# Kernel optimization log

Hardware: AMD Instinct MI355X
Metric: run time of the kernel (lower is better)

Reference implementation:

```python
import jax, jax.numpy as jnp
import numpy as np

ALPHA = 0.2  # LeakyReLU negative slope (args.alpha)

def _leaky(x):
    return jnp.where(x >= 0, x, ALPHA * x)

def setup_inputs() -> dict:
    key = jax.random.key(0)
    k1, k2, k3, k4 = jax.random.split(key, 4)
    B, N, F_in, F_out = 4, 2048, 512, 512
    h = jax.random.normal(k1, (B, N, F_in), dtype=jnp.float32)
    W = jax.random.normal(k2, (F_in, F_out), dtype=jnp.float32) * 0.05
    a = jax.random.normal(k3, (2 * F_out, 1), dtype=jnp.float32) * 0.05
    adj = jax.random.randint(k4, (B, N, N), 0, 2, dtype=jnp.int32)
    return {"h": h, "W": W, "a": a, "adj": adj}

def reference(h, W, a, adj):
    F_out = W.shape[1]
    Wh = jnp.matmul(h, W)                      # [B, N, F_out]
    # a_input is built under torch.no_grad() in the original -> stop_gradient
    Wh_sg = jax.lax.stop_gradient(Wh)
    a1 = a[:F_out, 0]                          # score for node i (repeat_interleave side)
    a2 = a[F_out:, 0]                          # score for node j (repeat side)
    s_i = Wh_sg @ a1                           # [B, N]
    s_j = Wh_sg @ a2                           # [B, N]
    e = _leaky(s_i[:, :, None] + s_j[:, None, :])   # [B, N, N]
    e = jnp.where(adj > 0, e, jnp.float32(-9e15))
    attention = jax.nn.softmax(e, axis=1)      # softmax over dim=1, as in original
    # dropout skipped (eval mode, training=False)
    h_prime = jnp.einsum('bij,bjf->bif', attention, Wh)
    return _leaky(h_prime)                     # concat=True
```

## Files before the change

### kernel.cpp

```cpp
#include <hip/hip_runtime.h>

#define BB 4
#define NN 2048
#define FF 512
#define ALPHA 0.2f

typedef unsigned short u16;
typedef unsigned int u32;
typedef __attribute__((ext_vector_type(8))) short bf16x8;
typedef __attribute__((ext_vector_type(4))) float f32x4;

__device__ __forceinline__ u16 f2bf(float x) {
  union { float f; u32 u; } v; v.f = x;
  u32 r = v.u + 0x7fffu + ((v.u >> 16) & 1u);
  return (u16)(r >> 16);
}
__device__ __forceinline__ float leaky(float x) { return x >= 0.f ? x : ALPHA * x; }

__global__ __launch_bounds__(256) void k_wa(const float* __restrict__ W,
                                            const float* __restrict__ a,
                                            float* __restrict__ wa1,
                                            float* __restrict__ wa2) {
  const int wave = threadIdx.x >> 6, lane = threadIdx.x & 63;
  const int k = blockIdx.x * 4 + wave;
  const int f0 = lane * 8;
  float4 w0 = *(const float4*)(W + (size_t)k * FF + f0);
  float4 w1 = *(const float4*)(W + (size_t)k * FF + f0 + 4);
  float4 p0 = *(const float4*)(a + f0);
  float4 p1 = *(const float4*)(a + f0 + 4);
  float4 q0 = *(const float4*)(a + FF + f0);
  float4 q1 = *(const float4*)(a + FF + f0 + 4);
  float d1 = w0.x*p0.x + w0.y*p0.y + w0.z*p0.z + w0.w*p0.w
           + w1.x*p1.x + w1.y*p1.y + w1.z*p1.z + w1.w*p1.w;
  float d2 = w0.x*q0.x + w0.y*q0.y + w0.z*q0.z + w0.w*q0.w
           + w1.x*q1.x + w1.y*q1.y + w1.z*q1.z + w1.w*q1.w;
#pragma unroll
  for (int o = 32; o; o >>= 1) { d1 += __shfl_xor(d1, o); d2 += __shfl_xor(d2, o); }
  if (lane == 0) { wa1[k] = d1; wa2[k] = d2; }
}

__global__ __launch_bounds__(256) void k_wt(const float* __restrict__ W,
                                            u16* __restrict__ wt) {
  __shared__ float T[64][65];
  const int k0 = blockIdx.x * 64, f0 = blockIdx.y * 64;
  const int tid = threadIdx.x;
  const int c = tid & 15, r0 = tid >> 4;
#pragma unroll
  for (int p = 0; p < 4; p++) {
    const int k = r0 + p * 16;
    float4 v = *(const float4*)(W + (size_t)(k0 + k) * FF + f0 + c * 4);
    T[c * 4 + 0][k] = v.x;
    T[c * 4 + 1][k] = v.y;
    T[c * 4 + 2][k] = v.z;
    T[c * 4 + 3][k] = v.w;
  }
  __syncthreads();
  const int kc = tid & 7, fr0 = tid >> 3;
#pragma unroll
  for (int p = 0; p < 2; p++) {
    const int f = fr0 + p * 32;
    union { uint4 q; u16 s[8]; } o;
#pragma unroll
    for (int q = 0; q < 8; q++) o.s[q] = f2bf(T[f][kc * 8 + q]);
    *(uint4*)(wt + (size_t)(f0 + f) * FF + k0 + kc * 8) = o.q;
  }
}

__global__ __launch_bounds__(256) void k_s(const float* __restrict__ h,
                                           const float* __restrict__ wa1,
                                           const float* __restrict__ wa2,
                                           float* __restrict__ s1,
                                           float* __restrict__ s2,
                                           u16* __restrict__ hbf) {
  const int wave = threadIdx.x >> 6, lane = threadIdx.x & 63;
  const int row = blockIdx.x * 4 + wave;
  const int f0 = lane * 8;
  float4 h0 = *(const float4*)(h + (size_t)row * FF + f0);
  float4 h1 = *(const float4*)(h + (size_t)row * FF + f0 + 4);
  float4 p0 = *(const float4*)(wa1 + f0);
  float4 p1 = *(const float4*)(wa1 + f0 + 4);
  float4 q0 = *(const float4*)(wa2 + f0);
  float4 q1 = *(const float4*)(wa2 + f0 + 4);
  union { uint4 q; u16 s[8]; } ob;
  ob.s[0] = f2bf(h0.x); ob.s[1] = f2bf(h0.y); ob.s[2] = f2bf(h0.z); ob.s[3] = f2bf(h0.w);
  ob.s[4] = f2bf(h1.x); ob.s[5] = f2bf(h1.y); ob.s[6] = f2bf(h1.z); ob.s[7] = f2bf(h1.w);
  *(uint4*)(hbf + (size_t)row * FF + f0) = ob.q;
  float d1 = h0.x*p0.x + h0.y*p0.y + h0.z*p0.z + h0.w*p0.w
           + h1.x*p1.x + h1.y*p1.y + h1.z*p1.z + h1.w*p1.w;
  float d2 = h0.x*q0.x + h0.y*q0.y + h0.z*q0.z + h0.w*q0.w
           + h1.x*q1.x + h1.y*q1.y + h1.z*q1.z + h1.w*q1.w;
#pragma unroll
  for (int o = 32; o; o >>= 1) { d1 += __shfl_xor(d1, o); d2 += __shfl_xor(d2, o); }
  if (lane == 0) { s1[row] = d1; s2[row] = d2; }
}

__global__ __launch_bounds__(512) void k_l(const int* __restrict__ adj,
                                           const float* __restrict__ s1,
                                           const float* __restrict__ s2,
                                           float* __restrict__ lpart,
                                           u16* __restrict__ P) {
  const int b = blockIdx.y, i0 = blockIdx.x * 16, t = threadIdx.x;
  const int j4 = t * 4;
  float4 s2v = *(const float4*)(s2 + b * NN + j4);
  float a0 = 0.f, a1 = 0.f, a2 = 0.f, a3 = 0.f;
  const int* abase = adj + ((size_t)b * NN + i0) * NN + j4;
  u16* pbase = P + ((size_t)b * NN + i0) * NN + j4;
#pragma unroll 4
  for (int i = 0; i < 16; i++) {
    int4 A = *(const int4*)(abase + (size_t)i * NN);
    const float s1i = s1[b * NN + i0 + i];
    float p0 = (A.x > 0) ? __expf(leaky(s1i + s2v.x)) : 0.f;
    float p1 = (A.y > 0) ? __expf(leaky(s1i + s2v.y)) : 0.f;
    float p2 = (A.z > 0) ? __expf(leaky(s1i + s2v.z)) : 0.f;
    float p3 = (A.w > 0) ? __expf(leaky(s1i + s2v.w)) : 0.f;
    a0 += p0; a1 += p1; a2 += p2; a3 += p3;
    ushort4 o; o.x = f2bf(p0); o.y = f2bf(p1); o.z = f2bf(p2); o.w = f2bf(p3);
    *(ushort4*)(pbase + (size_t)i * NN) = o;
  }
  float4 r; r.x = a0; r.y = a1; r.z = a2; r.w = a3;
  *(float4*)(lpart + (size_t)blockIdx.x * (BB * NN) + b * NN + j4) = r;
}

__global__ __launch_bounds__(256) void k_lred(const float* __restrict__ lpart,
                                              float* __restrict__ l) {
  const int idx = blockIdx.x * 256 + threadIdx.x;
  float s = 0.f;
#pragma unroll 8
  for (int c = 0; c < 128; c++) s += lpart[(size_t)c * (BB * NN) + idx];
  l[idx] = s;
}

__global__ __launch_bounds__(256) void k_wh(const u16* __restrict__ hbf,
                                            const u16* __restrict__ wt,
                                            const float* __restrict__ l,
                                            u16* __restrict__ whT) {
  __shared__ __attribute__((aligned(16))) u16 As[64][40];
  __shared__ __attribute__((aligned(16))) u16 Bs[128][40];
  const int m0 = blockIdx.x * 64, f0 = blockIdx.y * 128;
  const int tid = threadIdx.x, wave = tid >> 6, lane = tid & 63;
  const int wf = (wave >> 1) * 64, wi = (wave & 1) * 32;

  f32x4 acc[4][2];
#pragma unroll
  for (int x = 0; x < 4; x++)
#pragma unroll
    for (int y = 0; y < 2; y++) acc[x][y] = f32x4{0.f, 0.f, 0.f, 0.f};

  const int kc = tid & 3, ib = tid >> 2;
  for (int k0 = 0; k0 < FF; k0 += 32) {
    *(uint4*)(&As[ib][kc * 8]) =
        *(const uint4*)(hbf + (size_t)(m0 + ib) * FF + k0 + kc * 8);
#pragma unroll
    for (int p = 0; p < 2; p++) {
      const int f = ib + p * 64;
      *(uint4*)(&Bs[f][kc * 8]) =
          *(const uint4*)(wt + (size_t)(f0 + f) * FF + k0 + kc * 8);
    }
    __syncthreads();
    {
      const int r = lane & 15, kq = lane >> 4;
      bf16x8 wfr[4], hfr[2];
#pragma unroll
      for (int fi = 0; fi < 4; fi++) wfr[fi] = *(const bf16x8*)(&Bs[wf + fi * 16 + r][kq * 8]);
#pragma unroll
      for (int ii = 0; ii < 2; ii++) hfr[ii] = *(const bf16x8*)(&As[wi + ii * 16 + r][kq * 8]);
#pragma unroll
      for (int fi = 0; fi < 4; fi++)
#pragma unroll
        for (int ii = 0; ii < 2; ii++)
          acc[fi][ii] = __builtin_amdgcn_mfma_f32_16x16x32_bf16(wfr[fi], hfr[ii], acc[fi][ii], 0, 0, 0);
    }
    __syncthreads();
  }

  const int b = m0 >> 11, ibase = m0 & (NN - 1);
  const int r = lane & 15, rg = lane >> 4;
#pragma unroll
  for (int ii = 0; ii < 2; ii++) {
    const int icol = ibase + wi + ii * 16 + r;
    const float rl = __builtin_amdgcn_rcpf(l[b * NN + icol]);
#pragma unroll
    for (int fi = 0; fi < 4; fi++)
#pragma unroll
      for (int rr = 0; rr < 4; rr++) {
        const int f = f0 + wf + fi * 16 + rg * 4 + rr;
        whT[((size_t)b * FF + f) * NN + icol] = f2bf(acc[fi][ii][rr] * rl);
      }
  }
}

__global__ __launch_bounds__(512) void k_out(const u16* __restrict__ P,
                                             const u16* __restrict__ whS,
                                             float* __restrict__ out) {
  __shared__ __attribute__((aligned(16))) u16 As[2][128][64];
  __shared__ __attribute__((aligned(16))) u16 Bs[2][64][64];
  const int bid = blockIdx.x;
  const int L = (bid & 7) * 64 + (bid >> 3);
  const int b = L >> 7, it = (L >> 3) & 15, ft = L & 7;
  const int i0 = it * 128, f0 = ft * 64;
  const int tid = threadIdx.x, wave = tid >> 6, lane = tid & 63;
  const int wm = (wave >> 1) * 32, wn = (wave & 1) * 32;

  const int srow = lane >> 3;
  const int scol = (((lane & 7) ^ (srow & 7)) << 3);
  const u16* gA0 = P + ((size_t)(b * NN + i0 + wave * 16 + srow)) * NN + scol;
  const u16* gB0 = whS + ((size_t)(b * FF + f0 + wave * 8 + srow)) * NN + scol;

  f32x4 acc[2][2];
#pragma unroll
  for (int x = 0; x < 2; x++)
#pragma unroll
    for (int y = 0; y < 2; y++) acc[x][y] = f32x4{0.f, 0.f, 0.f, 0.f};

  auto STAGE = [&](int buf, int off16) {
#pragma unroll
    for (int p = 0; p < 2; p++)
      __builtin_amdgcn_global_load_lds(
          (const __attribute__((address_space(1))) void*)(gA0 + (size_t)p * 8 * NN + off16),
          (__attribute__((address_space(3))) void*)(&As[buf][wave * 16 + p * 8][0]), 16, 0, 0);
    __builtin_amdgcn_global_load_lds(
        (const __attribute__((address_space(1))) void*)(gB0 + off16),
        (__attribute__((address_space(3))) void*)(&Bs[buf][wave * 8][0]), 16, 0, 0);
  };

  STAGE(0, 0);

  int cur = 0;
  const int r = lane & 15, kq = lane >> 4;
  const int sx = (r & 7) << 3;
  for (int t = 0; t < 32; t++) {
    if (t < 31) {
      STAGE(cur ^ 1, (t + 1) * 64);
      asm volatile("s_waitcnt vmcnt(3)" ::: "memory");
    } else {
      asm volatile("s_waitcnt vmcnt(0)" ::: "memory");
    }
    __builtin_amdgcn_s_barrier();
#pragma unroll
    for (int kk = 0; kk < 2; kk++) {
      bf16x8 af[2], bv[2];
#pragma unroll
      for (int mi = 0; mi < 2; mi++)
        af[mi] = *(const bf16x8*)(&As[cur][wm + mi * 16 + r][(kk * 32 + kq * 8) ^ sx]);
#pragma unroll
      for (int ni = 0; ni < 2; ni++)
        bv[ni] = *(const bf16x8*)(&Bs[cur][wn + ni * 16 + r][(kk * 32 + kq * 8) ^ sx]);
#pragma unroll
      for (int mi = 0; mi < 2; mi++)
#pragma unroll
        for (int ni = 0; ni < 2; ni++)
          acc[mi][ni] = __builtin_amdgcn_mfma_f32_16x16x32_bf16(af[mi], bv[ni], acc[mi][ni], 0, 0, 0);
    }
    __builtin_amdgcn_s_barrier();
    cur ^= 1;
  }

  const int rg = lane >> 4;
#pragma unroll
  for (int mi = 0; mi < 2; mi++)
#pragma unroll
    for (int ni = 0; ni < 2; ni++) {
      const int f = f0 + wn + ni * 16 + r;
#pragma unroll
      for (int rr = 0; rr < 4; rr++) {
        const int i = i0 + wm + mi * 16 + rg * 4 + rr;
        out[((size_t)b * NN + i) * FF + f] = leaky(acc[mi][ni][rr]);
      }
    }
}

extern "C" void kernel_launch(void* const* d_in, const int* in_sizes, int n_in,
                              void* d_out, int out_size, void* d_ws, size_t ws_size,
                              hipStream_t stream) {
  const float* h = (const float*)d_in[0];
  const float* W = (const float*)d_in[1];
  const float* a = (const float*)d_in[2];
  const int* adj = (const int*)d_in[3];
  float* out = (float*)d_out;

  char* ws = (char*)d_ws;
  u16* whT = (u16*)ws;
  float* lpart = (float*)ws;
  u16* P = (u16*)(ws + (size_t)8388608);
  float* s1 = (float*)(ws + (size_t)8388608 + 33554432);
  float* s2 = s1 + BB * NN;
  float* lsum = s2 + BB * NN;
  float* wa1 = lsum + BB * NN;
  float* wa2 = wa1 + FF;
  u16* hbf = (u16*)(wa2 + FF);
  u16* wt = hbf + (size_t)BB * NN * FF;

  k_wa<<<dim3(128), 256, 0, stream>>>(W, a, wa1, wa2);
  k_wt<<<dim3(8, 8), 256, 0, stream>>>(W, wt);
  k_s<<<dim3(2048), 256, 0, stream>>>(h, wa1, wa2, s1, s2, hbf);
  k_l<<<dim3(128, 4), 512, 0, stream>>>(adj, s1, s2, lpart, P);
  k_lred<<<dim3(32), 256, 0, stream>>>(lpart, lsum);
  k_wh<<<dim3(128, 4), 256, 0, stream>>>(hbf, wt, lsum, whT);
  k_out<<<dim3(512), 512, 0, stream>>>(P, whT, out);
}
```

Measured before the change: 81.55 us.

## Pipeline k_wh with async LDS loads, widen k_l and shrink k_out waves

```diff
diff --git a/kernel.cpp b/kernel.cpp
--- a/kernel.cpp
+++ b/kernel.cpp
@@ -99,26 +99,36 @@
                                            const float* __restrict__ s2,
                                            float* __restrict__ lpart,
                                            u16* __restrict__ P) {
-  const int b = blockIdx.y, i0 = blockIdx.x * 16, t = threadIdx.x;
-  const int j4 = t * 4;
-  float4 s2v = *(const float4*)(s2 + b * NN + j4);
-  float a0 = 0.f, a1 = 0.f, a2 = 0.f, a3 = 0.f;
-  const int* abase = adj + ((size_t)b * NN + i0) * NN + j4;
-  u16* pbase = P + ((size_t)b * NN + i0) * NN + j4;
+  const int b = blockIdx.y, t = threadIdx.x;
+  const int rh = t >> 8;
+  const int tj = t & 255, j8 = tj * 8;
+  const int i0 = blockIdx.x * 16 + rh * 8;
+  float s2v[8];
+  *(float4*)(&s2v[0]) = *(const float4*)(s2 + b * NN + j8);
+  *(float4*)(&s2v[4]) = *(const float4*)(s2 + b * NN + j8 + 4);
+  float accv[8];
+#pragma unroll
+  for (int k = 0; k < 8; k++) accv[k] = 0.f;
+  const int* abase = adj + ((size_t)b * NN + i0) * NN + j8;
+  u16* pbase = P + ((size_t)b * NN + i0) * NN + j8;
 #pragma unroll 4
-  for (int i = 0; i < 16; i++) {
-    int4 A = *(const int4*)(abase + (size_t)i * NN);
+  for (int i = 0; i < 8; i++) {
+    int4 A0 = *(const int4*)(abase + (size_t)i * NN);
+    int4 A1 = *(const int4*)(abase + (size_t)i * NN + 4);
     const float s1i = s1[b * NN + i0 + i];
-    float p0 = (A.x > 0) ? __expf(leaky(s1i + s2v.x)) : 0.f;
-    float p1 = (A.y > 0) ? __expf(leaky(s1i + s2v.y)) : 0.f;
-    float p2 = (A.z > 0) ? __expf(leaky(s1i + s2v.z)) : 0.f;
-    float p3 = (A.w > 0) ? __expf(leaky(s1i + s2v.w)) : 0.f;
-    a0 += p0; a1 += p1; a2 += p2; a3 += p3;
-    ushort4 o; o.x = f2bf(p0); o.y = f2bf(p1); o.z = f2bf(p2); o.w = f2bf(p3);
-    *(ushort4*)(pbase + (size_t)i * NN) = o;
-  }
-  float4 r; r.x = a0; r.y = a1; r.z = a2; r.w = a3;
-  *(float4*)(lpart + (size_t)blockIdx.x * (BB * NN) + b * NN + j4) = r;
+    int av[8] = {A0.x, A0.y, A0.z, A0.w, A1.x, A1.y, A1.z, A1.w};
+    union { uint4 q; u16 s[8]; } o;
+#pragma unroll
+    for (int k = 0; k < 8; k++) {
+      float p = (av[k] > 0) ? __expf(leaky(s1i + s2v[k])) : 0.f;
+      accv[k] += p;
+      o.s[k] = f2bf(p);
+    }
+    *(uint4*)(pbase + (size_t)i * NN) = o.q;
+  }
+  float* lp = lpart + (size_t)(blockIdx.x * 2 + rh) * (BB * NN) + b * NN + j8;
+  *(float4*)lp = *(float4*)(&accv[0]);
+  *(float4*)(lp + 4) = *(float4*)(&accv[4]);
 }
 
 __global__ __launch_bounds__(256) void k_lred(const float* __restrict__ lpart,
@@ -126,7 +136,7 @@
   const int idx = blockIdx.x * 256 + threadIdx.x;
   float s = 0.f;
 #pragma unroll 8
-  for (int c = 0; c < 128; c++) s += lpart[(size_t)c * (BB * NN) + idx];
+  for (int c = 0; c < 256; c++) s += lpart[(size_t)c * (BB * NN) + idx];
   l[idx] = s;
 }
 
@@ -134,11 +144,21 @@
                                             const u16* __restrict__ wt,
                                             const float* __restrict__ l,
                                             u16* __restrict__ whT) {
-  __shared__ __attribute__((aligned(16))) u16 As[64][40];
-  __shared__ __attribute__((aligned(16))) u16 Bs[128][40];
-  const int m0 = blockIdx.x * 64, f0 = blockIdx.y * 128;
+  __shared__ __attribute__((aligned(16))) u16 As[2][128][64];
+  __shared__ __attribute__((aligned(16))) u16 Bs[2][64][64];
+  const int bid = blockIdx.x;
+  const int L = (bid & 7) * 64 + (bid >> 3);
+  const int it = L >> 2, ft = L & 3;
+  const int iG0 = it * 64;
+  const int b = iG0 >> 11, icol0 = iG0 & (NN - 1);
+  const int f0 = ft * 128;
   const int tid = threadIdx.x, wave = tid >> 6, lane = tid & 63;
-  const int wf = (wave >> 1) * 64, wi = (wave & 1) * 32;
+  const int wm = (wave >> 1) * 64, wn = (wave & 1) * 32;
+
+  const int srow = lane >> 3;
+  const int scol = (((lane & 7) ^ (srow & 7)) << 3);
+  const u16* gA0 = wt + ((size_t)(f0 + wave * 32 + srow)) * FF + scol;
+  const u16* gB0 = hbf + ((size_t)(iG0 + wave * 16 + srow)) * FF + scol;
 
   f32x4 acc[4][2];
 #pragma unroll
@@ -146,50 +166,68 @@
 #pragma unroll
     for (int y = 0; y < 2; y++) acc[x][y] = f32x4{0.f, 0.f, 0.f, 0.f};
 
-  const int kc = tid & 3, ib = tid >> 2;
-  for (int k0 = 0; k0 < FF; k0 += 32) {
-    *(uint4*)(&As[ib][kc * 8]) =
-        *(const uint4*)(hbf + (size_t)(m0 + ib) * FF + k0 + kc * 8);
-#pragma unroll
-    for (int p = 0; p < 2; p++) {
-      const int f = ib + p * 64;
-      *(uint4*)(&Bs[f][kc * 8]) =
-          *(const uint4*)(wt + (size_t)(f0 + f) * FF + k0 + kc * 8);
-    }
-    __syncthreads();
-    {
-      const int r = lane & 15, kq = lane >> 4;
-      bf16x8 wfr[4], hfr[2];
-#pragma unroll
-      for (int fi = 0; fi < 4; fi++) wfr[fi] = *(const bf16x8*)(&Bs[wf + fi * 16 + r][kq * 8]);
-#pragma unroll
-      for (int ii = 0; ii < 2; ii++) hfr[ii] = *(const bf16x8*)(&As[wi + ii * 16 + r][kq * 8]);
-#pragma unroll
-      for (int fi = 0; fi < 4; fi++)
-#pragma unroll
-        for (int ii = 0; ii < 2; ii++)
-          acc[fi][ii] = __builtin_amdgcn_mfma_f32_16x16x32_bf16(wfr[fi], hfr[ii], acc[fi][ii], 0, 0, 0);
-    }
-    __syncthreads();
-  }
-
-  const int b = m0 >> 11, ibase = m0 & (NN - 1);
-  const int r = lane & 15, rg = lane >> 4;
-#pragma unroll
-  for (int ii = 0; ii < 2; ii++) {
-    const int icol = ibase + wi + ii * 16 + r;
+  auto STAGE = [&](int buf, int off16) {
+#pragma unroll
+    for (int p = 0; p < 4; p++)
+      __builtin_amdgcn_global_load_lds(
+          (const __attribute__((address_space(1))) void*)(gA0 + (size_t)p * 8 * FF + off16),
+          (__attribute__((address_space(3))) void*)(&As[buf][wave * 32 + p * 8][0]), 16, 0, 0);
+#pragma unroll
+    for (int p = 0; p < 2; p++)
+      __builtin_amdgcn_global_load_lds(
+          (const __attribute__((address_space(1))) void*)(gB0 + (size_t)p * 8 * FF + off16),
+          (__attribute__((address_space(3))) void*)(&Bs[buf][wave * 16 + p * 8][0]), 16, 0, 0);
+  };
+
+  STAGE(0, 0);
+
+  int cur = 0;
+  const int r = lane & 15, kq = lane >> 4;
+  const int sx = (r & 7) << 3;
+  for (int t = 0; t < 8; t++) {
+    if (t < 7) {
+      STAGE(cur ^ 1, (t + 1) * 64);
+      asm volatile("s_waitcnt vmcnt(6)" ::: "memory");
+    } else {
+      asm volatile("s_waitcnt vmcnt(0)" ::: "memory");
+    }
+    __builtin_amdgcn_s_barrier();
+#pragma unroll
+    for (int kk = 0; kk < 2; kk++) {
+      bf16x8 af[4], bv[2];
+#pragma unroll
+      for (int mi = 0; mi < 4; mi++)
+        af[mi] = *(const bf16x8*)(&As[cur][wm + mi * 16 + r][(kk * 32 + kq * 8) ^ sx]);
+#pragma unroll
+      for (int ni = 0; ni < 2; ni++)
+        bv[ni] = *(const bf16x8*)(&Bs[cur][wn + ni * 16 + r][(kk * 32 + kq * 8) ^ sx]);
+#pragma unroll
+      for (int mi = 0; mi < 4; mi++)
+#pragma unroll
+        for (int ni = 0; ni < 2; ni++)
+          acc[mi][ni] = __builtin_amdgcn_mfma_f32_16x16x32_bf16(af[mi], bv[ni], acc[mi][ni], 0, 0, 0);
+    }
+    __builtin_amdgcn_s_barrier();
+    cur ^= 1;
+  }
+
+  const int rg = lane >> 4;
+#pragma unroll
+  for (int ni = 0; ni < 2; ni++) {
+    const int icol = icol0 + wn + ni * 16 + r;
     const float rl = __builtin_amdgcn_rcpf(l[b * NN + icol]);
 #pragma unroll
-    for (int fi = 0; fi < 4; fi++)
+    for (int mi = 0; mi < 4; mi++) {
 #pragma unroll
       for (int rr = 0; rr < 4; rr++) {
-        const int f = f0 + wf + fi * 16 + rg * 4 + rr;
-        whT[((size_t)b * FF + f) * NN + icol] = f2bf(acc[fi][ii][rr] * rl);
+        const int f = f0 + wm + mi * 16 + rg * 4 + rr;
+        whT[((size_t)b * FF + f) * NN + icol] = f2bf(acc[mi][ni][rr] * rl);
       }
-  }
-}
-
-__global__ __launch_bounds__(512) void k_out(const u16* __restrict__ P,
+    }
+  }
+}
+
+__global__ __launch_bounds__(256) void k_out(const u16* __restrict__ P,
                                              const u16* __restrict__ whS,
                                              float* __restrict__ out) {
   __shared__ __attribute__((aligned(16))) u16 As[2][128][64];
@@ -199,28 +237,30 @@
   const int b = L >> 7, it = (L >> 3) & 15, ft = L & 7;
   const int i0 = it * 128, f0 = ft * 64;
   const int tid = threadIdx.x, wave = tid >> 6, lane = tid & 63;
-  const int wm = (wave >> 1) * 32, wn = (wave & 1) * 32;
+  const int wm = (wave >> 1) * 64, wn = (wave & 1) * 32;
 
   const int srow = lane >> 3;
   const int scol = (((lane & 7) ^ (srow & 7)) << 3);
-  const u16* gA0 = P + ((size_t)(b * NN + i0 + wave * 16 + srow)) * NN + scol;
-  const u16* gB0 = whS + ((size_t)(b * FF + f0 + wave * 8 + srow)) * NN + scol;
-
-  f32x4 acc[2][2];
-#pragma unroll
-  for (int x = 0; x < 2; x++)
+  const u16* gA0 = P + ((size_t)(b * NN + i0 + wave * 32 + srow)) * NN + scol;
+  const u16* gB0 = whS + ((size_t)(b * FF + f0 + wave * 16 + srow)) * NN + scol;
+
+  f32x4 acc[4][2];
+#pragma unroll
+  for (int x = 0; x < 4; x++)
 #pragma unroll
     for (int y = 0; y < 2; y++) acc[x][y] = f32x4{0.f, 0.f, 0.f, 0.f};
 
   auto STAGE = [&](int buf, int off16) {
+#pragma unroll
+    for (int p = 0; p < 4; p++)
+      __builtin_amdgcn_global_load_lds(
+          (const __attribute__((address_space(1))) void*)(gA0 + (size_t)p * 8 * NN + off16),
+          (__attribute__((address_space(3))) void*)(&As[buf][wave * 32 + p * 8][0]), 16, 0, 0);
 #pragma unroll
     for (int p = 0; p < 2; p++)
       __builtin_amdgcn_global_load_lds(
-          (const __attribute__((address_space(1))) void*)(gA0 + (size_t)p * 8 * NN + off16),
-          (__attribute__((address_space(3))) void*)(&As[buf][wave * 16 + p * 8][0]), 16, 0, 0);
-    __builtin_amdgcn_global_load_lds(
-        (const __attribute__((address_space(1))) void*)(gB0 + off16),
-        (__attribute__((address_space(3))) void*)(&Bs[buf][wave * 8][0]), 16, 0, 0);
+          (const __attribute__((address_space(1))) void*)(gB0 + (size_t)p * 8 * NN + off16),
+          (__attribute__((address_space(3))) void*)(&Bs[buf][wave * 16 + p * 8][0]), 16, 0, 0);
   };
 
   STAGE(0, 0);
@@ -231,22 +271,22 @@
   for (int t = 0; t < 32; t++) {
     if (t < 31) {
       STAGE(cur ^ 1, (t + 1) * 64);
-      asm volatile("s_waitcnt vmcnt(3)" ::: "memory");
+      asm volatile("s_waitcnt vmcnt(6)" ::: "memory");
     } else {
       asm volatile("s_waitcnt vmcnt(0)" ::: "memory");
     }
     __builtin_amdgcn_s_barrier();
 #pragma unroll
     for (int kk = 0; kk < 2; kk++) {
-      bf16x8 af[2], bv[2];
-#pragma unroll
-      for (int mi = 0; mi < 2; mi++)
+      bf16x8 af[4], bv[2];
+#pragma unroll
+      for (int mi = 0; mi < 4; mi++)
         af[mi] = *(const bf16x8*)(&As[cur][wm + mi * 16 + r][(kk * 32 + kq * 8) ^ sx]);
 #pragma unroll
       for (int ni = 0; ni < 2; ni++)
         bv[ni] = *(const bf16x8*)(&Bs[cur][wn + ni * 16 + r][(kk * 32 + kq * 8) ^ sx]);
 #pragma unroll
-      for (int mi = 0; mi < 2; mi++)
+      for (int mi = 0; mi < 4; mi++)
 #pragma unroll
         for (int ni = 0; ni < 2; ni++)
           acc[mi][ni] = __builtin_amdgcn_mfma_f32_16x16x32_bf16(af[mi], bv[ni], acc[mi][ni], 0, 0, 0);
@@ -257,7 +297,7 @@
 
   const int rg = lane >> 4;
 #pragma unroll
-  for (int mi = 0; mi < 2; mi++)
+  for (int mi = 0; mi < 4; mi++)
 #pragma unroll
     for (int ni = 0; ni < 2; ni++) {
       const int f = f0 + wn + ni * 16 + r;
@@ -295,6 +335,6 @@
   k_s<<<dim3(2048), 256, 0, stream>>>(h, wa1, wa2, s1, s2, hbf);
   k_l<<<dim3(128, 4), 512, 0, stream>>>(adj, s1, s2, lpart, P);
   k_lred<<<dim3(32), 256, 0, stream>>>(lpart, lsum);
-  k_wh<<<dim3(128, 4), 256, 0, stream>>>(hbf, wt, lsum, whT);
-  k_out<<<dim3(512), 512, 0, stream>>>(P, whT, out);
-}
+  k_wh<<<dim3(512), 256, 0, stream>>>(hbf, wt, lsum, whT);
+  k_out<<<dim3(512), 256, 0, stream>>>(P, whT, out);
+}
```

Result: slower. 86.62 us (+6.2%).
